# Performance work log

Measured on AMD Instinct MI355X. Metric: run time of the kernel, lower is better.

## Reference

```python
import jax, jax.numpy as jnp
import numpy as np

N, E, D, H = 50000, 600000, 128, 128
SLOPE = 0.01  # default negative_slope of F.leaky_relu / nn.LeakyReLU


def leaky(x):
    return jnp.where(x >= 0, x, SLOPE * x)


def gcn_conv(x, src, dst, W, b, n):
    """PyG GCNConv: x' = D^{-1/2}(A+I)D^{-1/2} (x W) + b, symmetric norm with self-loops."""
    h = x @ W  # [n, out]
    ones = jnp.ones(src.shape[0], h.dtype)
    deg = jax.ops.segment_sum(ones, dst, num_segments=n) + 1.0  # +1 for self-loop
    dinv = jax.lax.rsqrt(deg)  # deg >= 1 always
    norm = dinv[src] * dinv[dst]  # per-edge coefficient
    msg = h[src] * norm[:, None]  # gather + scale: [E, out]
    agg = jax.ops.segment_sum(msg, dst, num_segments=n)  # scatter-add
    agg = agg + h * (dinv * dinv)[:, None]  # self-loop term
    return agg + b


def setup_inputs() -> dict:
    key = jax.random.key(0)
    ks = jax.random.split(key, 16)
    kaiming = lambda k, fi, fo: jax.random.normal(k, (fi, fo), jnp.float32) * np.sqrt(2.0 / fi)
    return {
        "x": jax.random.normal(ks[0], (N, D), jnp.float32),
        "edge_index": jax.random.randint(ks[1], (2, E), 0, N, jnp.int64 if jax.config.jax_enable_x64 else jnp.int32),
        "gen_data": jax.random.normal(ks[2], (N, H), jnp.float32),
        "Wc1": kaiming(ks[3], D, H), "bc1": jnp.zeros((H,), jnp.float32),
        "Wc2": kaiming(ks[4], H, H), "bc2": jnp.zeros((H,), jnp.float32),
        "Wm1": kaiming(ks[5], H, H), "bm1": jnp.zeros((H,), jnp.float32),
        "Wm2": kaiming(ks[6], H, H), "bm2": jnp.zeros((H,), jnp.float32),
        "Wp1": kaiming(ks[7], H, H), "bp1": jnp.zeros((H,), jnp.float32),
        "Wp2": kaiming(ks[8], H, H), "bp2": jnp.zeros((H,), jnp.float32),
    }


def reference(x, edge_index, gen_data, Wc1, bc1, Wc2, bc2, Wm1, bm1, Wm2, bm2, Wp1, bp1, Wp2, bp2):
    src, dst = edge_index[0], edge_index[1]
    lambd = 0.5
    # GraphEncoder4Link
    h = leaky(gcn_conv(x, src, dst, Wc1, bc1, N))
    h = leaky(gcn_conv(h, src, dst, Wc2, bc2, N) + h)
    h = leaky((leaky(h @ Wm1 + bm1) @ Wm2 + bm2) + h)
    # lambd interpolation with gen_data
    out = lambd * h + (1.0 - lambd) * gen_data
    # proj MLP
    out = leaky(leaky(out @ Wp1 + bp1) @ Wp2 + bp2)
    return out
```

## Files before the change

kernel.cpp:

```cpp
#include <hip/hip_runtime.h>
#include <cstdint>
#include <cstddef>

#define HH 128
#define SLOPE 0.01f

typedef __attribute__((ext_vector_type(8))) __bf16 bf16x8;
typedef __attribute__((ext_vector_type(8))) unsigned short ushort8v;
typedef __attribute__((ext_vector_type(4))) float f32x4;

__device__ __forceinline__ float lrelu(float x) { return x >= 0.f ? x : SLOPE * x; }
__device__ __forceinline__ unsigned short f2b(float f) {
  union { float f; unsigned u; } v; v.f = f;
  unsigned r = v.u + 0x7fffu + ((v.u >> 16) & 1u);
  return (unsigned short)(r >> 16);
}
__device__ __forceinline__ float b2f(unsigned short u) {
  union { unsigned u; float f; } v; v.u = ((unsigned)u) << 16; return v.f;
}

__device__ __forceinline__ int lofs(int r, int k) {
  return (r << 7) + ((((k >> 3) ^ r) & 15) << 3) + (k & 7);
}

#define WAVE_SYNC() asm volatile("s_waitcnt lgkmcnt(0)" ::: "memory")


__global__ __launch_bounds__(256) void count_kernel(const int* __restrict__ dst,
                                                    int* __restrict__ cnt, int nE) {
  int e = blockIdx.x * 256 + threadIdx.x;
  if (e < nE) atomicAdd(&cnt[dst[e]], 1);
}

__global__ __launch_bounds__(1024) void scan1_kernel(int* __restrict__ cnt,
                                                     int* __restrict__ rowptr,
                                                     int* __restrict__ bsum,
                                                     float* __restrict__ dinv, int n) {
  __shared__ int wsum[16];
  const int tid = threadIdx.x;
  const int lane = tid & 63, wid = tid >> 6;
  int i = blockIdx.x * 1024 + tid;
  int v = (i < n) ? cnt[i] : 0;
  int x = v;
#pragma unroll
  for (int off = 1; off < 64; off <<= 1) {
    int y = __shfl_up(x, off, 64);
    if (lane >= off) x += y;
  }
  if (lane == 63) wsum[wid] = x;
  __syncthreads();
  if (tid == 0) {
    int s = 0;
#pragma unroll
    for (int w = 0; w < 16; ++w) { int t = wsum[w]; wsum[w] = s; s += t; }
    bsum[blockIdx.x] = s;
  }
  __syncthreads();
  if (i < n) {
    rowptr[i] = wsum[wid] + x - v;
    dinv[i] = rsqrtf((float)v + 1.0f);
    cnt[i] = 0;
  }
}

__global__ __launch_bounds__(64) void scan2_kernel(int* __restrict__ bsum, int nb,
                                                   int* __restrict__ rowptr, int n, int E) {
  int lane = threadIdx.x;
  int v = (lane < nb) ? bsum[lane] : 0;
  int x = v;
#pragma unroll
  for (int off = 1; off < 64; off <<= 1) {
    int y = __shfl_up(x, off, 64);
    if (lane >= off) x += y;
  }
  if (lane < nb) bsum[lane] = x - v;
  if (lane == 0) rowptr[n] = E;
}

__global__ __launch_bounds__(1024) void scan3_kernel(int* __restrict__ rowptr,
                                                     const int* __restrict__ bsum, int n) {
  int i = blockIdx.x * 1024 + threadIdx.x;
  if (i < n) rowptr[i] += bsum[blockIdx.x];
}

__global__ __launch_bounds__(256) void fill_kernel(const int* __restrict__ src,
                                                   const int* __restrict__ dst,
                                                   const int* __restrict__ rowptr,
                                                   int* __restrict__ cursor,
                                                   const float* __restrict__ dinv,
                                                   int2* __restrict__ csr, int nE) {
  int e = blockIdx.x * 256 + threadIdx.x;
  if (e >= nE) return;
  int d = dst[e], s = src[e];
  int pos = rowptr[d] + atomicAdd(&cursor[d], 1);
  int2 ent;
  ent.x = s;
  ent.y = __float_as_int(dinv[s] * dinv[d]);
  csr[pos] = ent;
}

__global__ __launch_bounds__(256) void pack_kernel(const float* W0, const float* W1,
                                                   const float* W2, const float* W3,
                                                   const float* W4, const float* W5,
                                                   unsigned short* __restrict__ out) {
  const float* Ws[6] = {W0, W1, W2, W3, W4, W5};
  const float* W = Ws[blockIdx.y];
  int f = blockIdx.x * 256 + threadIdx.x;
  int j = f & 7, L = (f >> 3) & 63, c = (f >> 9) & 7, t = f >> 12;
  int k = t * 32 + (L >> 4) * 8 + j;
  int n = c * 16 + (L & 15);
  out[(size_t)blockIdx.y * 16384 + f] = f2b(W[k * HH + n]);
}


__device__ __forceinline__ void mfma_stage(const unsigned short* __restrict__ Alds,
                                           const bf16x8* __restrict__ Wf,
                                           int arow, int lane, int quad, f32x4* acc) {
#pragma unroll
  for (int c = 0; c < 8; ++c) acc[c] = (f32x4){0.f, 0.f, 0.f, 0.f};
#pragma unroll
  for (int t = 0; t < 4; ++t) {
    bf16x8 a = *(const bf16x8*)&Alds[lofs(arow, t * 32 + quad * 8)];
#pragma unroll
    for (int c = 0; c < 8; ++c)
      acc[c] = __builtin_amdgcn_mfma_f32_16x16x32_bf16(a, Wf[(t * 8 + c) * 64 + lane], acc[c], 0, 0, 0);
  }
}


__global__ __launch_bounds__(64) void gemm_conv(const float* __restrict__ A,
                                                const unsigned short* __restrict__ Wp,
                                                unsigned short* __restrict__ out, int nrows) {
  const int lane = threadIdx.x;
  const int row0 = blockIdx.x * 16;
  const int m = lane & 15, quad = lane >> 4;
  const int gr = row0 + m;
  const bool rok = gr < nrows;
  const float* Arow = A + (size_t)gr * HH;
  const bf16x8* Wf = (const bf16x8*)Wp;

  bf16x8 af[4];
#pragma unroll
  for (int t = 0; t < 4; ++t) {
    const int k = t * 32 + quad * 8;
    float4 lo = make_float4(0.f, 0.f, 0.f, 0.f), hi = lo;
    if (rok) {
      lo = *(const float4*)(Arow + k);
      hi = *(const float4*)(Arow + k + 4);
    }
    union { ushort8v u; bf16x8 b; } cv;
    cv.u[0] = f2b(lo.x); cv.u[1] = f2b(lo.y); cv.u[2] = f2b(lo.z); cv.u[3] = f2b(lo.w);
    cv.u[4] = f2b(hi.x); cv.u[5] = f2b(hi.y); cv.u[6] = f2b(hi.z); cv.u[7] = f2b(hi.w);
    af[t] = cv.b;
  }

  f32x4 acc[8];
#pragma unroll
  for (int c = 0; c < 8; ++c) acc[c] = (f32x4){0.f, 0.f, 0.f, 0.f};
#pragma unroll
  for (int t = 0; t < 4; ++t)
#pragma unroll
    for (int c = 0; c < 8; ++c)
      acc[c] = __builtin_amdgcn_mfma_f32_16x16x32_bf16(af[t], Wf[(t * 8 + c) * 64 + lane], acc[c], 0, 0, 0);

#pragma unroll
  for (int c = 0; c < 8; ++c) {
    int col = c * 16 + m;
#pragma unroll
    for (int g = 0; g < 4; ++g) {
      int row = row0 + quad * 4 + g;
      if (row < nrows) out[(size_t)row * HH + col] = f2b(acc[c][g]);
    }
  }
}


template <int RES, int OUTBF>
__global__ __launch_bounds__(256) void agg_kernel(const unsigned short* __restrict__ h,
                                                  const int* __restrict__ rowptr,
                                                  const int2* __restrict__ csr,
                                                  const float* __restrict__ dinv,
                                                  const float* __restrict__ bias,
                                                  const float* __restrict__ res,
                                                  void* __restrict__ outv, int n) {
  int node = blockIdx.x * 4 + (threadIdx.x >> 6);
  if (node >= n) return;
  int lane = threadIdx.x & 63;
  int c = lane << 1;
  int j = rowptr[node], end = rowptr[node + 1];
  float ax = 0.f, ay = 0.f;
  for (; j + 8 <= end; j += 8) {
    int2 e[8];
    ushort2 r[8];
#pragma unroll
    for (int q = 0; q < 8; ++q) e[q] = csr[j + q];
#pragma unroll
    for (int q = 0; q < 8; ++q) r[q] = *(const ushort2*)(h + (size_t)e[q].x * HH + c);
#pragma unroll
    for (int q = 0; q < 8; ++q) {
      float nv = __int_as_float(e[q].y);
      ax = fmaf(b2f(r[q].x), nv, ax); ay = fmaf(b2f(r[q].y), nv, ay);
    }
  }
  for (; j + 2 <= end; j += 2) {
    int2 e0 = csr[j], e1 = csr[j + 1];
    ushort2 r0 = *(const ushort2*)(h + (size_t)e0.x * HH + c);
    ushort2 r1 = *(const ushort2*)(h + (size_t)e1.x * HH + c);
    float n0 = __int_as_float(e0.y), n1 = __int_as_float(e1.y);
    ax = fmaf(b2f(r0.x), n0, ax); ay = fmaf(b2f(r0.y), n0, ay);
    ax = fmaf(b2f(r1.x), n1, ax); ay = fmaf(b2f(r1.y), n1, ay);
  }
  if (j < end) {
    int2 e0 = csr[j];
    float n0 = __int_as_float(e0.y);
    ushort2 r0 = *(const ushort2*)(h + (size_t)e0.x * HH + c);
    ax = fmaf(b2f(r0.x), n0, ax); ay = fmaf(b2f(r0.y), n0, ay);
  }
  float di = dinv[node], d2 = di * di;
  ushort2 hs = *(const ushort2*)(h + (size_t)node * HH + c);
  float2 b = *(const float2*)(bias + c);
  float ox = ax + b2f(hs.x) * d2 + b.x;
  float oy = ay + b2f(hs.y) * d2 + b.y;
  if (RES) {
    float2 r = *(const float2*)(res + (size_t)node * HH + c);
    ox += r.x; oy += r.y;
  }
  ox = lrelu(ox); oy = lrelu(oy);
  if (OUTBF) {
    ushort2 o; o.x = f2b(ox); o.y = f2b(oy);
    *(ushort2*)((unsigned short*)outv + (size_t)node * HH + c) = o;
  } else {
    *(float2*)((float*)outv + (size_t)node * HH + c) = make_float2(ox, oy);
  }
}


__global__ __launch_bounds__(64) void fusedMLP(const unsigned short* __restrict__ f2bf,
                                               const unsigned short* __restrict__ Wm1p,
                                               const unsigned short* __restrict__ Wm2p,
                                               const unsigned short* __restrict__ Wp1p,
                                               const unsigned short* __restrict__ Wp2p,
                                               const float* __restrict__ bm1,
                                               const float* __restrict__ bm2,
                                               const float* __restrict__ bp1,
                                               const float* __restrict__ bp2,
                                               const float* __restrict__ gen,
                                               float* __restrict__ out, int n) {
  __shared__ __align__(16) unsigned short Al[16 * HH];
  __shared__ __align__(16) unsigned short Bl[16 * HH];
  const int lane = threadIdx.x;
  const int row0 = blockIdx.x * 16;
  const int m = lane & 15, quad = lane >> 4;

#pragma unroll
  for (int i = 0; i < 4; ++i) {
    int idx = i * 64 + lane;
    int r = idx >> 4, k = (idx & 15) << 3;
    int gr = row0 + r;
    ushort8v v = {0, 0, 0, 0, 0, 0, 0, 0};
    if (gr < n) v = *(const ushort8v*)(f2bf + (size_t)gr * HH + k);
    *(ushort8v*)&Al[lofs(r, k)] = v;
  }

  float genv[8][4];
#pragma unroll
  for (int cc = 0; cc < 8; ++cc)
#pragma unroll
    for (int g = 0; g < 4; ++g) {
      int grow = row0 + quad * 4 + g;
      genv[cc][g] = (grow < n) ? gen[(size_t)grow * HH + cc * 16 + m] : 0.f;
    }

  f32x4 acc[8];
  WAVE_SYNC();

  float b1v[8];
#pragma unroll
  for (int cc = 0; cc < 8; ++cc) b1v[cc] = bm1[cc * 16 + m];
  mfma_stage(Al, (const bf16x8*)Wm1p, m, lane, quad, acc);
#pragma unroll
  for (int cc = 0; cc < 8; ++cc) {
    int col = cc * 16 + m;
#pragma unroll
    for (int g = 0; g < 4; ++g) {
      int lrow = quad * 4 + g;
      Bl[lofs(lrow, col)] = f2b(lrelu(acc[cc][g] + b1v[cc]));
    }
  }
  WAVE_SYNC();

  float b2v[8];
#pragma unroll
  for (int cc = 0; cc < 8; ++cc) b2v[cc] = bm2[cc * 16 + m];
  mfma_stage(Bl, (const bf16x8*)Wm2p, m, lane, quad, acc);
#pragma unroll
  for (int cc = 0; cc < 8; ++cc) {
    int col = cc * 16 + m;
#pragma unroll
    for (int g = 0; g < 4; ++g) {
      int lrow = quad * 4 + g;
      float f2v = b2f(Al[lofs(lrow, col)]);
      float v = lrelu(acc[cc][g] + b2v[cc] + f2v);
      Al[lofs(lrow, col)] = f2b(0.5f * (v + genv[cc][g]));
    }
  }
  WAVE_SYNC();

  float b3v[8];
#pragma unroll
  for (int cc = 0; cc < 8; ++cc) b3v[cc] = bp1[cc * 16 + m];
  mfma_stage(Al, (const bf16x8*)Wp1p, m, lane, quad, acc);
#pragma unroll
  for (int cc = 0; cc < 8; ++cc) {
    int col = cc * 16 + m;
#pragma unroll
    for (int g = 0; g < 4; ++g) {
      int lrow = quad * 4 + g;
      Bl[lofs(lrow, col)] = f2b(lrelu(acc[cc][g] + b3v[cc]));
    }
  }
  WAVE_SYNC();

  float b4v[8];
#pragma unroll
  for (int cc = 0; cc < 8; ++cc) b4v[cc] = bp2[cc * 16 + m];
  mfma_stage(Bl, (const bf16x8*)Wp2p, m, lane, quad, acc);
#pragma unroll
  for (int cc = 0; cc < 8; ++cc) {
    int col = cc * 16 + m;
#pragma unroll
    for (int g = 0; g < 4; ++g) {
      int row = row0 + quad * 4 + g;
      if (row < n) out[(size_t)row * HH + col] = lrelu(acc[cc][g] + b4v[cc]);
    }
  }
}


extern "C" void kernel_launch(void* const* d_in, const int* in_sizes, int n_in,
                              void* d_out, int out_size, void* d_ws, size_t ws_size,
                              hipStream_t stream) {
  const float* x   = (const float*)d_in[0];
  const int* ei    = (const int*)d_in[1];
  const float* gen = (const float*)d_in[2];
  const float* Wc1 = (const float*)d_in[3];
  const float* bc1 = (const float*)d_in[4];
  const float* Wc2 = (const float*)d_in[5];
  const float* bc2 = (const float*)d_in[6];
  const float* Wm1 = (const float*)d_in[7];
  const float* bm1 = (const float*)d_in[8];
  const float* Wm2 = (const float*)d_in[9];
  const float* bm2 = (const float*)d_in[10];
  const float* Wp1 = (const float*)d_in[11];
  const float* bp1 = (const float*)d_in[12];
  const float* Wp2 = (const float*)d_in[13];
  const float* bp2 = (const float*)d_in[14];

  const int N = in_sizes[0] / HH;
  const int E = in_sizes[1] / 2;
  const int* src = ei;
  const int* dst = ei + E;

  char* ws = (char*)d_ws;
  size_t off = 0;
  auto alloc = [&](size_t bytes) { void* p = ws + off; off += (bytes + 255) & ~(size_t)255; return p; };
  float* dinv            = (float*)alloc((size_t)N * 4);
  int*   rowptr          = (int*)  alloc((size_t)(N + 1) * 4);
  int*   cursor          = (int*)  alloc((size_t)N * 4);
  int*   bsum            = (int*)  alloc((size_t)64 * 4);
  int2*  csr             = (int2*) alloc((size_t)E * 8);
  unsigned short* h_bf   = (unsigned short*)alloc((size_t)N * HH * 2);
  unsigned short* t2_bf  = (unsigned short*)alloc((size_t)N * HH * 2);
  unsigned short* f2_bf  = (unsigned short*)alloc((size_t)N * HH * 2);
  float* f1_f32          = (float*)alloc((size_t)N * HH * 4);
  unsigned short* packed = (unsigned short*)alloc((size_t)6 * 16384 * 2);
  float* fOut = (float*)d_out;

  const int wblocks = (N + 15) / 16;
  const int eblocks = (E + 255) / 256;
  const int ablocks = (N + 3) / 4;
  const int sblocks = (N + 1023) / 1024;

  pack_kernel<<<dim3(64, 6), 256, 0, stream>>>(Wc1, Wc2, Wm1, Wm2, Wp1, Wp2, packed);

  hipMemsetAsync(cursor, 0, (size_t)N * 4, stream);
  count_kernel<<<eblocks, 256, 0, stream>>>(dst, cursor, E);
  scan1_kernel<<<sblocks, 1024, 0, stream>>>(cursor, rowptr, bsum, dinv, N);
  scan2_kernel<<<1, 64, 0, stream>>>(bsum, sblocks, rowptr, N, E);
  scan3_kernel<<<sblocks, 1024, 0, stream>>>(rowptr, bsum, N);
  fill_kernel<<<eblocks, 256, 0, stream>>>(src, dst, rowptr, cursor, dinv, csr, E);

  gemm_conv<<<wblocks, 64, 0, stream>>>(x, packed + 0 * 16384, h_bf, N);
  agg_kernel<0, 0><<<ablocks, 256, 0, stream>>>(h_bf, rowptr, csr, dinv, bc1, nullptr, f1_f32, N);
  gemm_conv<<<wblocks, 64, 0, stream>>>(f1_f32, packed + 1 * 16384, t2_bf, N);
  agg_kernel<1, 1><<<ablocks, 256, 0, stream>>>(t2_bf, rowptr, csr, dinv, bc2, f1_f32, f2_bf, N);
  fusedMLP<<<wblocks, 64, 0, stream>>>(f2_bf,
                                       packed + 2 * 16384, packed + 3 * 16384,
                                       packed + 4 * 16384, packed + 5 * 16384,
                                       bm1, bm2, bp1, bp2, gen, fOut, N);
}
```

Before: 301.0 us.

## Process 32 rows per wave in GEMM kernels to reuse weight fragments

The dense GEMM and fused MLP kernels now handle two 16-row tiles per wavefront, loading each weight fragment once into registers and applying it to both tiles. This halves weight traffic per row and halves the block count. The gen_data values are also packed into bf16 pairs to save registers. The cost is much higher register pressure (acc[2][8], wf[16], af[2][4]), which may reduce occupancy or cause spills, and gen is now rounded to bf16 before blending, a small precision change.

```diff
diff --git a/kernel.cpp b/kernel.cpp
--- a/kernel.cpp
+++ b/kernel.cpp
@@ -113,65 +113,84 @@
 }
 
 
-__device__ __forceinline__ void mfma_stage(const unsigned short* __restrict__ Alds,
-                                           const bf16x8* __restrict__ Wf,
-                                           int arow, int lane, int quad, f32x4* acc) {
-#pragma unroll
-  for (int c = 0; c < 8; ++c) acc[c] = (f32x4){0.f, 0.f, 0.f, 0.f};
-#pragma unroll
-  for (int t = 0; t < 4; ++t) {
-    bf16x8 a = *(const bf16x8*)&Alds[lofs(arow, t * 32 + quad * 8)];
-#pragma unroll
-    for (int c = 0; c < 8; ++c)
-      acc[c] = __builtin_amdgcn_mfma_f32_16x16x32_bf16(a, Wf[(t * 8 + c) * 64 + lane], acc[c], 0, 0, 0);
-  }
-}
-
-
-__global__ __launch_bounds__(64) void gemm_conv(const float* __restrict__ A,
-                                                const unsigned short* __restrict__ Wp,
-                                                unsigned short* __restrict__ out, int nrows) {
+__device__ __forceinline__ void mfma_w32(const bf16x8 af[2][4], const bf16x8* __restrict__ Wf,
+                                         int lane, f32x4 acc[2][8]) {
+#pragma unroll
+  for (int tt = 0; tt < 2; ++tt)
+#pragma unroll
+    for (int c = 0; c < 8; ++c) acc[tt][c] = (f32x4){0.f, 0.f, 0.f, 0.f};
+#pragma unroll
+  for (int h = 0; h < 2; ++h) {
+    bf16x8 wf[16];
+#pragma unroll
+    for (int i = 0; i < 16; ++i) wf[i] = Wf[(h * 16 + i) * 64 + lane];
+#pragma unroll
+    for (int th = 0; th < 2; ++th) {
+      const int t = h * 2 + th;
+#pragma unroll
+      for (int c = 0; c < 8; ++c) {
+#pragma unroll
+        for (int tt = 0; tt < 2; ++tt)
+          acc[tt][c] = __builtin_amdgcn_mfma_f32_16x16x32_bf16(af[tt][t], wf[th * 8 + c],
+                                                               acc[tt][c], 0, 0, 0);
+      }
+    }
+  }
+}
+
+__device__ __forceinline__ void lds_afrags(const unsigned short* __restrict__ Tl,
+                                           int m, int quad, bf16x8 af[2][4]) {
+#pragma unroll
+  for (int tt = 0; tt < 2; ++tt)
+#pragma unroll
+    for (int t = 0; t < 4; ++t)
+      af[tt][t] = *(const bf16x8*)&Tl[lofs(tt * 16 + m, t * 32 + quad * 8)];
+}
+
+
+__global__ __launch_bounds__(64, 2) void gemm_conv(const float* __restrict__ A,
+                                                   const unsigned short* __restrict__ Wp,
+                                                   unsigned short* __restrict__ out, int nrows) {
   const int lane = threadIdx.x;
-  const int row0 = blockIdx.x * 16;
+  const int row0 = blockIdx.x * 32;
   const int m = lane & 15, quad = lane >> 4;
-  const int gr = row0 + m;
-  const bool rok = gr < nrows;
-  const float* Arow = A + (size_t)gr * HH;
   const bf16x8* Wf = (const bf16x8*)Wp;
 
-  bf16x8 af[4];
-#pragma unroll
-  for (int t = 0; t < 4; ++t) {
-    const int k = t * 32 + quad * 8;
-    float4 lo = make_float4(0.f, 0.f, 0.f, 0.f), hi = lo;
-    if (rok) {
-      lo = *(const float4*)(Arow + k);
-      hi = *(const float4*)(Arow + k + 4);
-    }
-    union { ushort8v u; bf16x8 b; } cv;
-    cv.u[0] = f2b(lo.x); cv.u[1] = f2b(lo.y); cv.u[2] = f2b(lo.z); cv.u[3] = f2b(lo.w);
-    cv.u[4] = f2b(hi.x); cv.u[5] = f2b(hi.y); cv.u[6] = f2b(hi.z); cv.u[7] = f2b(hi.w);
-    af[t] = cv.b;
-  }
-
-  f32x4 acc[8];
-#pragma unroll
-  for (int c = 0; c < 8; ++c) acc[c] = (f32x4){0.f, 0.f, 0.f, 0.f};
-#pragma unroll
-  for (int t = 0; t < 4; ++t)
-#pragma unroll
-    for (int c = 0; c < 8; ++c)
-      acc[c] = __builtin_amdgcn_mfma_f32_16x16x32_bf16(af[t], Wf[(t * 8 + c) * 64 + lane], acc[c], 0, 0, 0);
-
-#pragma unroll
-  for (int c = 0; c < 8; ++c) {
-    int col = c * 16 + m;
-#pragma unroll
-    for (int g = 0; g < 4; ++g) {
-      int row = row0 + quad * 4 + g;
-      if (row < nrows) out[(size_t)row * HH + col] = f2b(acc[c][g]);
-    }
-  }
+  bf16x8 af[2][4];
+#pragma unroll
+  for (int tt = 0; tt < 2; ++tt) {
+    const int gr = row0 + tt * 16 + m;
+    const bool rok = gr < nrows;
+    const float* Arow = A + (size_t)gr * HH;
+#pragma unroll
+    for (int t = 0; t < 4; ++t) {
+      const int k = t * 32 + quad * 8;
+      float4 lo = make_float4(0.f, 0.f, 0.f, 0.f), hi = lo;
+      if (rok) {
+        lo = *(const float4*)(Arow + k);
+        hi = *(const float4*)(Arow + k + 4);
+      }
+      union { ushort8v u; bf16x8 b; } cv;
+      cv.u[0] = f2b(lo.x); cv.u[1] = f2b(lo.y); cv.u[2] = f2b(lo.z); cv.u[3] = f2b(lo.w);
+      cv.u[4] = f2b(hi.x); cv.u[5] = f2b(hi.y); cv.u[6] = f2b(hi.z); cv.u[7] = f2b(hi.w);
+      af[tt][t] = cv.b;
+    }
+  }
+
+  f32x4 acc[2][8];
+  mfma_w32(af, Wf, lane, acc);
+
+#pragma unroll
+  for (int tt = 0; tt < 2; ++tt)
+#pragma unroll
+    for (int c = 0; c < 8; ++c) {
+      int col = c * 16 + m;
+#pragma unroll
+      for (int g = 0; g < 4; ++g) {
+        int row = row0 + tt * 16 + quad * 4 + g;
+        if (row < nrows) out[(size_t)row * HH + col] = f2b(acc[tt][c][g]);
+      }
+    }
 }
 
 
@@ -235,25 +254,25 @@
 }
 
 
-__global__ __launch_bounds__(64) void fusedMLP(const unsigned short* __restrict__ f2bf,
-                                               const unsigned short* __restrict__ Wm1p,
-                                               const unsigned short* __restrict__ Wm2p,
-                                               const unsigned short* __restrict__ Wp1p,
-                                               const unsigned short* __restrict__ Wp2p,
-                                               const float* __restrict__ bm1,
-                                               const float* __restrict__ bm2,
-                                               const float* __restrict__ bp1,
-                                               const float* __restrict__ bp2,
-                                               const float* __restrict__ gen,
-                                               float* __restrict__ out, int n) {
-  __shared__ __align__(16) unsigned short Al[16 * HH];
-  __shared__ __align__(16) unsigned short Bl[16 * HH];
+__global__ __launch_bounds__(64, 2) void fusedMLP(const unsigned short* __restrict__ f2bf,
+                                                  const unsigned short* __restrict__ Wm1p,
+                                                  const unsigned short* __restrict__ Wm2p,
+                                                  const unsigned short* __restrict__ Wp1p,
+                                                  const unsigned short* __restrict__ Wp2p,
+                                                  const float* __restrict__ bm1,
+                                                  const float* __restrict__ bm2,
+                                                  const float* __restrict__ bp1,
+                                                  const float* __restrict__ bp2,
+                                                  const float* __restrict__ gen,
+                                                  float* __restrict__ out, int n) {
+  __shared__ __align__(16) unsigned short Al[32 * HH];
+  __shared__ __align__(16) unsigned short Bl[32 * HH];
   const int lane = threadIdx.x;
-  const int row0 = blockIdx.x * 16;
+  const int row0 = blockIdx.x * 32;
   const int m = lane & 15, quad = lane >> 4;
 
 #pragma unroll
-  for (int i = 0; i < 4; ++i) {
+  for (int i = 0; i < 8; ++i) {
     int idx = i * 64 + lane;
     int r = idx >> 4, k = (idx & 15) << 3;
     int gr = row0 + r;
@@ -262,78 +281,97 @@
     *(ushort8v*)&Al[lofs(r, k)] = v;
   }
 
-  float genv[8][4];
-#pragma unroll
-  for (int cc = 0; cc < 8; ++cc)
-#pragma unroll
-    for (int g = 0; g < 4; ++g) {
-      int grow = row0 + quad * 4 + g;
-      genv[cc][g] = (grow < n) ? gen[(size_t)grow * HH + cc * 16 + m] : 0.f;
-    }
-
-  f32x4 acc[8];
+  unsigned genp[2][8][2];
+#pragma unroll
+  for (int tt = 0; tt < 2; ++tt)
+#pragma unroll
+    for (int cc = 0; cc < 8; ++cc)
+#pragma unroll
+      for (int gp = 0; gp < 2; ++gp) {
+        int r0r = row0 + tt * 16 + quad * 4 + gp * 2;
+        float v0 = (r0r < n) ? gen[(size_t)r0r * HH + cc * 16 + m] : 0.f;
+        float v1 = (r0r + 1 < n) ? gen[(size_t)(r0r + 1) * HH + cc * 16 + m] : 0.f;
+        genp[tt][cc][gp] = (unsigned)f2b(v0) | ((unsigned)f2b(v1) << 16);
+      }
+
+  bf16x8 af[2][4];
+  f32x4 acc[2][8];
   WAVE_SYNC();
 
   float b1v[8];
 #pragma unroll
   for (int cc = 0; cc < 8; ++cc) b1v[cc] = bm1[cc * 16 + m];
-  mfma_stage(Al, (const bf16x8*)Wm1p, m, lane, quad, acc);
-#pragma unroll
-  for (int cc = 0; cc < 8; ++cc) {
-    int col = cc * 16 + m;
-#pragma unroll
-    for (int g = 0; g < 4; ++g) {
-      int lrow = quad * 4 + g;
-      Bl[lofs(lrow, col)] = f2b(lrelu(acc[cc][g] + b1v[cc]));
-    }
-  }
+  lds_afrags(Al, m, quad, af);
+  mfma_w32(af, (const bf16x8*)Wm1p, lane, acc);
+#pragma unroll
+  for (int tt = 0; tt < 2; ++tt)
+#pragma unroll
+    for (int cc = 0; cc < 8; ++cc) {
+      int col = cc * 16 + m;
+#pragma unroll
+      for (int g = 0; g < 4; ++g) {
+        int lrow = tt * 16 + quad * 4 + g;
+        Bl[lofs(lrow, col)] = f2b(lrelu(acc[tt][cc][g] + b1v[cc]));
+      }
+    }
   WAVE_SYNC();
 
   float b2v[8];
 #pragma unroll
   for (int cc = 0; cc < 8; ++cc) b2v[cc] = bm2[cc * 16 + m];
-  mfma_stage(Bl, (const bf16x8*)Wm2p, m, lane, quad, acc);
-#pragma unroll
-  for (int cc = 0; cc < 8; ++cc) {
-    int col = cc * 16 + m;
-#pragma unroll
-    for (int g = 0; g < 4; ++g) {
-      int lrow = quad * 4 + g;
-      float f2v = b2f(Al[lofs(lrow, col)]);
-      float v = lrelu(acc[cc][g] + b2v[cc] + f2v);
-      Al[lofs(lrow, col)] = f2b(0.5f * (v + genv[cc][g]));
-    }
-  }
+  lds_afrags(Bl, m, quad, af);
+  mfma_w32(af, (const bf16x8*)Wm2p, lane, acc);
+#pragma unroll
+  for (int tt = 0; tt < 2; ++tt)
+#pragma unroll
+    for (int cc = 0; cc < 8; ++cc) {
+      int col = cc * 16 + m;
+#pragma unroll
+      for (int g = 0; g < 4; ++g) {
+        int lrow = tt * 16 + quad * 4 + g;
+        float f2v = b2f(Al[lofs(lrow, col)]);
+        float v = lrelu(acc[tt][cc][g] + b2v[cc] + f2v);
+        unsigned gp = genp[tt][cc][g >> 1];
+        float gv = b2f((unsigned short)((g & 1) ? (gp >> 16) : (gp & 0xffffu)));
+        Al[lofs(lrow, col)] = f2b(0.5f * (v + gv));
+      }
+    }
   WAVE_SYNC();
 
   float b3v[8];
 #pragma unroll
   for (int cc = 0; cc < 8; ++cc) b3v[cc] = bp1[cc * 16 + m];
-  mfma_stage(Al, (const bf16x8*)Wp1p, m, lane, quad, acc);
-#pragma unroll
-  for (int cc = 0; cc < 8; ++cc) {
-    int col = cc * 16 + m;
-#pragma unroll
-    for (int g = 0; g < 4; ++g) {
-      int lrow = quad * 4 + g;
-      Bl[lofs(lrow, col)] = f2b(lrelu(acc[cc][g] + b3v[cc]));
-    }
-  }
+  lds_afrags(Al, m, quad, af);
+  mfma_w32(af, (const bf16x8*)Wp1p, lane, acc);
+#pragma unroll
+  for (int tt = 0; tt < 2; ++tt)
+#pragma unroll
+    for (int cc = 0; cc < 8; ++cc) {
+      int col = cc * 16 + m;
+#pragma unroll
+      for (int g = 0; g < 4; ++g) {
+        int lrow = tt * 16 + quad * 4 + g;
+        Bl[lofs(lrow, col)] = f2b(lrelu(acc[tt][cc][g] + b3v[cc]));
+      }
+    }
   WAVE_SYNC();
 
   float b4v[8];
 #pragma unroll
   for (int cc = 0; cc < 8; ++cc) b4v[cc] = bp2[cc * 16 + m];
-  mfma_stage(Bl, (const bf16x8*)Wp2p, m, lane, quad, acc);
-#pragma unroll
-  for (int cc = 0; cc < 8; ++cc) {
-    int col = cc * 16 + m;
-#pragma unroll
-    for (int g = 0; g < 4; ++g) {
-      int row = row0 + quad * 4 + g;
-      if (row < n) out[(size_t)row * HH + col] = lrelu(acc[cc][g] + b4v[cc]);
-    }
-  }
+  lds_afrags(Bl, m, quad, af);
+  mfma_w32(af, (const bf16x8*)Wp2p, lane, acc);
+#pragma unroll
+  for (int tt = 0; tt < 2; ++tt)
+#pragma unroll
+    for (int cc = 0; cc < 8; ++cc) {
+      int col = cc * 16 + m;
+#pragma unroll
+      for (int g = 0; g < 4; ++g) {
+        int row = row0 + tt * 16 + quad * 4 + g;
+        if (row < n) out[(size_t)row * HH + col] = lrelu(acc[tt][cc][g] + b4v[cc]);
+      }
+    }
 }
 
 
@@ -376,7 +414,7 @@
   unsigned short* packed = (unsigned short*)alloc((size_t)6 * 16384 * 2);
   float* fOut = (float*)d_out;
 
-  const int wblocks = (N + 15) / 16;
+  const int wblocks = (N + 31) / 32;
   const int eblocks = (E + 255) / 256;
   const int ablocks = (N + 3) / 4;
   const int sblocks = (N + 1023) / 1024;
```

After: 302.9 us. No clear change (+0.6%).

## Use 4-wave blocks for GEMM/MLP kernels, stage gen and biases to cut registers

Applied to the files above, without the earlier changes.

The conv GEMM and fused MLP kernels go from one 16-row wave per block to four independent waves per 256-thread block, each with its own LDS tiles. In the MLP, the gen_data tile is now stored as bf16 and passed through LDS rather than held as 32 fp32 registers, and all four bias vectors are staged once into LDS. Weight fragments are loaded into a small register batch before each group of MFMAs. The aim is lower register pressure and fewer tiny blocks so more waves stay resident, in exchange for more LDS per block, a bf16 rounding of gen_data, and __launch_bounds__(256,1), which may limit the compiler's occupancy target.

```diff
diff --git a/kernel.cpp b/kernel.cpp
--- a/kernel.cpp
+++ b/kernel.cpp
@@ -113,31 +113,39 @@
 }
 
 
-__device__ __forceinline__ void mfma_stage(const unsigned short* __restrict__ Alds,
-                                           const bf16x8* __restrict__ Wf,
-                                           int arow, int lane, int quad, f32x4* acc) {
+__device__ __forceinline__ void mfma_stage(const bf16x8 af[4], const bf16x8* __restrict__ Wf,
+                                           int lane, f32x4 acc[8]) {
 #pragma unroll
   for (int c = 0; c < 8; ++c) acc[c] = (f32x4){0.f, 0.f, 0.f, 0.f};
 #pragma unroll
   for (int t = 0; t < 4; ++t) {
-    bf16x8 a = *(const bf16x8*)&Alds[lofs(arow, t * 32 + quad * 8)];
+    bf16x8 wf[8];
+#pragma unroll
+    for (int c = 0; c < 8; ++c) wf[c] = Wf[(t * 8 + c) * 64 + lane];
 #pragma unroll
     for (int c = 0; c < 8; ++c)
-      acc[c] = __builtin_amdgcn_mfma_f32_16x16x32_bf16(a, Wf[(t * 8 + c) * 64 + lane], acc[c], 0, 0, 0);
-  }
-}
-
-
-__global__ __launch_bounds__(64) void gemm_conv(const float* __restrict__ A,
-                                                const unsigned short* __restrict__ Wp,
-                                                unsigned short* __restrict__ out, int nrows) {
-  const int lane = threadIdx.x;
-  const int row0 = blockIdx.x * 16;
+      acc[c] = __builtin_amdgcn_mfma_f32_16x16x32_bf16(af[t], wf[c], acc[c], 0, 0, 0);
+  }
+}
+
+__device__ __forceinline__ void lds_afrags16(const unsigned short* __restrict__ Tl,
+                                             int m, int quad, bf16x8 af[4]) {
+#pragma unroll
+  for (int t = 0; t < 4; ++t)
+    af[t] = *(const bf16x8*)&Tl[lofs(m, t * 32 + quad * 8)];
+}
+
+
+__global__ __launch_bounds__(256, 1) void gemm_conv(const float* __restrict__ A,
+                                                    const unsigned short* __restrict__ Wp,
+                                                    unsigned short* __restrict__ out, int nrows) {
+  const int tid = threadIdx.x;
+  const int lane = tid & 63, wave = tid >> 6;
+  const int row0 = blockIdx.x * 64 + wave * 16;
   const int m = lane & 15, quad = lane >> 4;
   const int gr = row0 + m;
   const bool rok = gr < nrows;
   const float* Arow = A + (size_t)gr * HH;
-  const bf16x8* Wf = (const bf16x8*)Wp;
 
   bf16x8 af[4];
 #pragma unroll
@@ -155,13 +163,7 @@
   }
 
   f32x4 acc[8];
-#pragma unroll
-  for (int c = 0; c < 8; ++c) acc[c] = (f32x4){0.f, 0.f, 0.f, 0.f};
-#pragma unroll
-  for (int t = 0; t < 4; ++t)
-#pragma unroll
-    for (int c = 0; c < 8; ++c)
-      acc[c] = __builtin_amdgcn_mfma_f32_16x16x32_bf16(af[t], Wf[(t * 8 + c) * 64 + lane], acc[c], 0, 0, 0);
+  mfma_stage(af, (const bf16x8*)Wp, lane, acc);
 
 #pragma unroll
   for (int c = 0; c < 8; ++c) {
@@ -235,22 +237,27 @@
 }
 
 
-__global__ __launch_bounds__(64) void fusedMLP(const unsigned short* __restrict__ f2bf,
-                                               const unsigned short* __restrict__ Wm1p,
-                                               const unsigned short* __restrict__ Wm2p,
-                                               const unsigned short* __restrict__ Wp1p,
-                                               const unsigned short* __restrict__ Wp2p,
-                                               const float* __restrict__ bm1,
-                                               const float* __restrict__ bm2,
-                                               const float* __restrict__ bp1,
-                                               const float* __restrict__ bp2,
-                                               const float* __restrict__ gen,
-                                               float* __restrict__ out, int n) {
-  __shared__ __align__(16) unsigned short Al[16 * HH];
-  __shared__ __align__(16) unsigned short Bl[16 * HH];
-  const int lane = threadIdx.x;
-  const int row0 = blockIdx.x * 16;
+__global__ __launch_bounds__(256, 1) void fusedMLP(const unsigned short* __restrict__ f2bf,
+                                                   const unsigned short* __restrict__ Wm1p,
+                                                   const unsigned short* __restrict__ Wm2p,
+                                                   const unsigned short* __restrict__ Wp1p,
+                                                   const unsigned short* __restrict__ Wp2p,
+                                                   const float* __restrict__ bm1,
+                                                   const float* __restrict__ bm2,
+                                                   const float* __restrict__ bp1,
+                                                   const float* __restrict__ bp2,
+                                                   const float* __restrict__ gen,
+                                                   float* __restrict__ out, int n) {
+  __shared__ __align__(16) unsigned short Ta[4][16 * HH];
+  __shared__ __align__(16) unsigned short Tb[4][16 * HH];
+  __shared__ __align__(16) float Bi[4][4 * HH];
+  const int tid = threadIdx.x;
+  const int lane = tid & 63, wave = tid >> 6;
+  const int row0 = blockIdx.x * 64 + wave * 16;
   const int m = lane & 15, quad = lane >> 4;
+  unsigned short* TA = Ta[wave];
+  unsigned short* TB = Tb[wave];
+  float* BI = Bi[wave];
 
 #pragma unroll
   for (int i = 0; i < 4; ++i) {
@@ -259,79 +266,98 @@
     int gr = row0 + r;
     ushort8v v = {0, 0, 0, 0, 0, 0, 0, 0};
     if (gr < n) v = *(const ushort8v*)(f2bf + (size_t)gr * HH + k);
-    *(ushort8v*)&Al[lofs(r, k)] = v;
-  }
-
-  float genv[8][4];
-#pragma unroll
-  for (int cc = 0; cc < 8; ++cc)
-#pragma unroll
-    for (int g = 0; g < 4; ++g) {
-      int grow = row0 + quad * 4 + g;
-      genv[cc][g] = (grow < n) ? gen[(size_t)grow * HH + cc * 16 + m] : 0.f;
-    }
-
+    *(ushort8v*)&TA[lofs(r, k)] = v;
+  }
+
+  ushort4 genb[8];
+#pragma unroll
+  for (int i = 0; i < 8; ++i) {
+    int idx = i * 64 + lane;
+    int r = idx >> 5, c4 = (idx & 31) << 2;
+    int gr = row0 + r;
+    float4 v = make_float4(0.f, 0.f, 0.f, 0.f);
+    if (gr < n) v = *(const float4*)(gen + (size_t)gr * HH + c4);
+    genb[i].x = f2b(v.x); genb[i].y = f2b(v.y); genb[i].z = f2b(v.z); genb[i].w = f2b(v.w);
+  }
+
+  {
+    const float* b01 = (lane < 32) ? bm1 : bm2;
+    const float* b23 = (lane < 32) ? bp1 : bp2;
+    int col = (lane & 31) << 2;
+    float4 v0 = *(const float4*)(b01 + col);
+    float4 v1 = *(const float4*)(b23 + col);
+    *(float4*)&BI[lane * 4] = v0;
+    *(float4*)&BI[256 + lane * 4] = v1;
+  }
+  WAVE_SYNC();
+
+  bf16x8 af[4];
   f32x4 acc[8];
-  WAVE_SYNC();
-
-  float b1v[8];
-#pragma unroll
-  for (int cc = 0; cc < 8; ++cc) b1v[cc] = bm1[cc * 16 + m];
-  mfma_stage(Al, (const bf16x8*)Wm1p, m, lane, quad, acc);
+  float bv[8];
+
+#pragma unroll
+  for (int cc = 0; cc < 8; ++cc) bv[cc] = BI[cc * 16 + m];
+  lds_afrags16(TA, m, quad, af);
+  mfma_stage(af, (const bf16x8*)Wm1p, lane, acc);
 #pragma unroll
   for (int cc = 0; cc < 8; ++cc) {
     int col = cc * 16 + m;
 #pragma unroll
-    for (int g = 0; g < 4; ++g) {
-      int lrow = quad * 4 + g;
-      Bl[lofs(lrow, col)] = f2b(lrelu(acc[cc][g] + b1v[cc]));
-    }
-  }
-  WAVE_SYNC();
-
-  float b2v[8];
-#pragma unroll
-  for (int cc = 0; cc < 8; ++cc) b2v[cc] = bm2[cc * 16 + m];
-  mfma_stage(Bl, (const bf16x8*)Wm2p, m, lane, quad, acc);
+    for (int g = 0; g < 4; ++g)
+      TB[lofs(quad * 4 + g, col)] = f2b(lrelu(acc[cc][g] + bv[cc]));
+  }
+  WAVE_SYNC();
+
+#pragma unroll
+  for (int cc = 0; cc < 8; ++cc) bv[cc] = BI[128 + cc * 16 + m];
+  lds_afrags16(TB, m, quad, af);
+  WAVE_SYNC();
+#pragma unroll
+  for (int i = 0; i < 8; ++i) {
+    int idx = i * 64 + lane;
+    int r = idx >> 5, c4 = (idx & 31) << 2;
+    *(ushort4*)&TB[lofs(r, c4)] = genb[i];
+  }
+  mfma_stage(af, (const bf16x8*)Wm2p, lane, acc);
+  WAVE_SYNC();
 #pragma unroll
   for (int cc = 0; cc < 8; ++cc) {
     int col = cc * 16 + m;
 #pragma unroll
     for (int g = 0; g < 4; ++g) {
-      int lrow = quad * 4 + g;
-      float f2v = b2f(Al[lofs(lrow, col)]);
-      float v = lrelu(acc[cc][g] + b2v[cc] + f2v);
-      Al[lofs(lrow, col)] = f2b(0.5f * (v + genv[cc][g]));
+      int lr = quad * 4 + g;
+      float f2v = b2f(TA[lofs(lr, col)]);
+      float v = lrelu(acc[cc][g] + bv[cc] + f2v);
+      float gv = b2f(TB[lofs(lr, col)]);
+      TA[lofs(lr, col)] = f2b(0.5f * (v + gv));
     }
   }
   WAVE_SYNC();
 
-  float b3v[8];
-#pragma unroll
-  for (int cc = 0; cc < 8; ++cc) b3v[cc] = bp1[cc * 16 + m];
-  mfma_stage(Al, (const bf16x8*)Wp1p, m, lane, quad, acc);
+#pragma unroll
+  for (int cc = 0; cc < 8; ++cc) bv[cc] = BI[256 + cc * 16 + m];
+  lds_afrags16(TA, m, quad, af);
+  mfma_stage(af, (const bf16x8*)Wp1p, lane, acc);
 #pragma unroll
   for (int cc = 0; cc < 8; ++cc) {
     int col = cc * 16 + m;
 #pragma unroll
-    for (int g = 0; g < 4; ++g) {
-      int lrow = quad * 4 + g;
-      Bl[lofs(lrow, col)] = f2b(lrelu(acc[cc][g] + b3v[cc]));
-    }
-  }
-  WAVE_SYNC();
-
-  float b4v[8];
-#pragma unroll
-  for (int cc = 0; cc < 8; ++cc) b4v[cc] = bp2[cc * 16 + m];
-  mfma_stage(Bl, (const bf16x8*)Wp2p, m, lane, quad, acc);
+    for (int g = 0; g < 4; ++g)
+      TB[lofs(quad * 4 + g, col)] = f2b(lrelu(acc[cc][g] + bv[cc]));
+  }
+  WAVE_SYNC();
+
+#pragma unroll
+  for (int cc = 0; cc < 8; ++cc) bv[cc] = BI[384 + cc * 16 + m];
+  lds_afrags16(TB, m, quad, af);
+  mfma_stage(af, (const bf16x8*)Wp2p, lane, acc);
 #pragma unroll
   for (int cc = 0; cc < 8; ++cc) {
     int col = cc * 16 + m;
 #pragma unroll
     for (int g = 0; g < 4; ++g) {
       int row = row0 + quad * 4 + g;
-      if (row < n) out[(size_t)row * HH + col] = lrelu(acc[cc][g] + b4v[cc]);
+      if (row < n) out[(size_t)row * HH + col] = lrelu(acc[cc][g] + bv[cc]);
     }
   }
 }
@@ -376,7 +402,7 @@
   unsigned short* packed = (unsigned short*)alloc((size_t)6 * 16384 * 2);
   float* fOut = (float*)d_out;
 
-  const int wblocks = (N + 15) / 16;
+  const int cblocks = (N + 63) / 64;
   const int eblocks = (E + 255) / 256;
   const int ablocks = (N + 3) / 4;
   const int sblocks = (N + 1023) / 1024;
@@ -390,12 +416,12 @@
   scan3_kernel<<<sblocks, 1024, 0, stream>>>(rowptr, bsum, N);
   fill_kernel<<<eblocks, 256, 0, stream>>>(src, dst, rowptr, cursor, dinv, csr, E);
 
-  gemm_conv<<<wblocks, 64, 0, stream>>>(x, packed + 0 * 16384, h_bf, N);
+  gemm_conv<<<cblocks, 256, 0, stream>>>(x, packed + 0 * 16384, h_bf, N);
   agg_kernel<0, 0><<<ablocks, 256, 0, stream>>>(h_bf, rowptr, csr, dinv, bc1, nullptr, f1_f32, N);
-  gemm_conv<<<wblocks, 64, 0, stream>>>(f1_f32, packed + 1 * 16384, t2_bf, N);
+  gemm_conv<<<cblocks, 256, 0, stream>>>(f1_f32, packed + 1 * 16384, t2_bf, N);
   agg_kernel<1, 1><<<ablocks, 256, 0, stream>>>(t2_bf, rowptr, csr, dinv, bc2, f1_f32, f2_bf, N);
-  fusedMLP<<<wblocks, 64, 0, stream>>>(f2_bf,
-                                       packed + 2 * 16384, packed + 3 * 16384,
-                                       packed + 4 * 16384, packed + 5 * 16384,
-                                       bm1, bm2, bp1, bp2, gen, fOut, N);
-}
+  fusedMLP<<<cblocks, 256, 0, stream>>>(f2_bf,
+                                        packed + 2 * 16384, packed + 3 * 16384,
+                                        packed + 4 * 16384, packed + 5 * 16384,
+                                        bm1, bm2, bp1, bp2, gen, fOut, N);
+}
```

Result: no change. 300.3 us (-0.2%).
